# Performance work log

Measured on AMD Instinct MI355X. Metric: run time of the kernel, lower is better.

Reference implementation:

```python
import jax, jax.numpy as jnp
import numpy as np

M, N = 32, 32          # grid size (input_size)
D = 8                  # input_dim
H = 64                 # hidden_dim
O = 1                  # output_dim
B = 8                  # batch
AVG_DEG = 32           # average in-degree of the grid graph


def _build_graph_edges():
    """Host-side (numpy) construction of the sparse grid graph and edge lists,
    mirroring GraphLSTM.__construct_net: self-edge first for every node, then
    every j with graph[i, j] != 0 (after |g| < 0.5 thresholding)."""
    rng = np.random.RandomState(0)
    MN = M * N
    keep = rng.rand(MN, MN) < (AVG_DEG / MN)
    sign = rng.choice([-1.0, 1.0], size=(MN, MN))
    mag = rng.uniform(0.5, 1.0, size=(MN, MN))  # magnitudes survive threshold
    graph = np.where(keep, sign * mag, 0.0).astype(np.float32)
    graph[(-0.5 < graph) & (graph < 0.5)] = 0.0  # faithful thresholding
    dst_nz, src_nz = np.nonzero(graph)
    # self edges are always present (weight = graph[i, i], possibly 0)
    self_idx = np.arange(MN)
    dst = np.concatenate([self_idx, dst_nz]).astype(np.int32)
    src = np.concatenate([self_idx, src_nz]).astype(np.int32)
    w = np.concatenate([np.diagonal(graph), graph[dst_nz, src_nz]]).astype(np.float32)
    return dst, src, w


def setup_inputs() -> dict:
    key = jax.random.key(0)
    k_x, k_wih, k_bih, k_bhh, k_cw, k_cb = jax.random.split(key, 6)
    dst_np, src_np, w_np = _build_graph_edges()
    E = dst_np.shape[0]
    scale = 0.05
    return {
        "x": jax.random.normal(k_x, (B, D, M, N), dtype=jnp.float32),
        "edge_w": jnp.asarray(w_np),                     # (E,)
        "W_ih": jax.random.normal(k_wih, (E, 4 * H, D), dtype=jnp.float32) * scale,
        "b_ih": jax.random.normal(k_bih, (E, 4 * H), dtype=jnp.float32) * scale,
        "b_hh": jax.random.normal(k_bhh, (E, 4 * H), dtype=jnp.float32) * scale,
        "conv_w": jax.random.normal(k_cw, (O, H), dtype=jnp.float32) * scale,
        "conv_b": jax.random.normal(k_cb, (O,), dtype=jnp.float32) * scale,
        "src_idx": jnp.asarray(src_np),                  # (E,) int32
        "dst_idx": jnp.asarray(dst_np),                  # (E,) int32
    }


def reference(x, edge_w, W_ih, b_ih, b_hh, conv_w, conv_b, src_idx, dst_idx):
    Bb, Dd, Mm, Nn = x.shape
    MN = Mm * Nn
    xf = x.reshape(Bb, Dd, MN)
    # gather per-edge source features: (B, D, E)
    x_src = xf[:, :, src_idx]
    # per-edge distinct LSTM cell, single step from zero state:
    # gates = x @ W_ih^T + b_ih + (W_hh @ h0 == 0) + b_hh
    gates = jnp.einsum('bde,egd->beg', x_src, W_ih) + b_ih + b_hh  # (B, E, 4H)
    i_g, f_g, g_g, o_g = jnp.split(gates, 4, axis=-1)  # torch LSTM gate order i,f,g,o
    c_new = jax.nn.sigmoid(i_g) * jnp.tanh(g_g)        # c0 = 0 => forget path drops
    h_new = jax.nn.sigmoid(o_g) * jnp.tanh(c_new)      # (B, E, H)
    # weighted scatter-sum over destination nodes
    wh = edge_w[None, :, None] * h_new                  # (B, E, H)
    node = jax.ops.segment_sum(jnp.swapaxes(wh, 0, 1), dst_idx, num_segments=MN)  # (MN, B, H)
    frame = jnp.transpose(node, (1, 2, 0)).reshape(Bb, H, Mm, Nn)  # (B, H, M, N)
    # 1x1 conv: hidden -> output channels
    out = jnp.einsum('bhmn,oh->bomn', frame, conv_w) + conv_b[None, :, None, None]
    return out
```

## Files before the change

### kernel.cpp

```cpp
#include <hip/hip_runtime.h>
#include <hip/hip_bf16.h>


#define MN 1024
#define BB 8
#define NCOPY 32

__device__ __forceinline__ float fsig(float x) {
    return __builtin_amdgcn_rcpf(1.0f + __expf(-x));
}
__device__ __forceinline__ float ftanh(float x) {
    float t = fminf(fmaxf(2.0f * x, -30.0f), 30.0f);
    float e = __expf(t);
    return (e - 1.0f) * __builtin_amdgcn_rcpf(e + 1.0f);
}
__device__ __forceinline__ float rl(float v, int idx) {
    return __int_as_float(__builtin_amdgcn_readlane(__float_as_int(v), idx));
}

__global__ void prep_kernel(const float* __restrict__ x,
                            float* __restrict__ xt,
                            float* __restrict__ partial) {
    int tid = blockIdx.x * 256 + threadIdx.x;
    if (tid < MN * BB * 8) {
        int mn = tid >> 6;
        int b  = (tid >> 3) & 7;
        int d  = tid & 7;
        xt[tid] = x[b * (8 * MN) + d * MN + mn];
    }
    float4* p4 = (float4*)partial;
    p4[tid] = make_float4(0.f, 0.f, 0.f, 0.f);
}

__global__ void reduce_kernel(const float* __restrict__ partial,
                              const float* __restrict__ conv_b,
                              float* __restrict__ out) {
    int tid = blockIdx.x * 256 + threadIdx.x;
    float s = conv_b[0];
#pragma unroll
    for (int k = 0; k < NCOPY; ++k) s += partial[k * (BB * MN) + tid];
    out[tid] = s;
}

struct WRegs {
    float4 wi0, wi1, wg0, wg1, wo0, wo1;
    float  bIi, bIh, bGi, bGh, bOi, bOh;
};

__device__ __forceinline__ void loadW(WRegs& r, int e, int lane,
        const float* __restrict__ W, const float* __restrict__ b_ih,
        const float* __restrict__ b_hh) {
    const float* We = W + (size_t)e * 2048 + lane * 8;
    r.wi0 = *(const float4*)(We);
    r.wi1 = *(const float4*)(We + 4);
    r.wg0 = *(const float4*)(We + 1024);
    r.wg1 = *(const float4*)(We + 1028);
    r.wo0 = *(const float4*)(We + 1536);
    r.wo1 = *(const float4*)(We + 1540);
    const float* bi = b_ih + (size_t)e * 256 + lane;
    const float* bh = b_hh + (size_t)e * 256 + lane;
    r.bIi = bi[0];   r.bIh = bh[0];
    r.bGi = bi[128]; r.bGh = bh[128];
    r.bOi = bi[192]; r.bOh = bh[192];
}

__device__ __forceinline__ void computeEdge(const WRegs& r, float xreg,
        int dst, float ew, float cw, float* __restrict__ pout, int lane) {
    float bI = r.bIi + r.bIh;
    float bG = r.bGi + r.bGh;
    float bO = r.bOi + r.bOh;
    float s[BB];
#pragma unroll
    for (int b = 0; b < BB; ++b) {
        float x0 = rl(xreg, b * 8 + 0), x1 = rl(xreg, b * 8 + 1);
        float x2 = rl(xreg, b * 8 + 2), x3 = rl(xreg, b * 8 + 3);
        float x4 = rl(xreg, b * 8 + 4), x5 = rl(xreg, b * 8 + 5);
        float x6 = rl(xreg, b * 8 + 6), x7 = rl(xreg, b * 8 + 7);
        float pi = bI, pg = bG, po = bO;
        pi = fmaf(r.wi0.x, x0, pi); pg = fmaf(r.wg0.x, x0, pg); po = fmaf(r.wo0.x, x0, po);
        pi = fmaf(r.wi0.y, x1, pi); pg = fmaf(r.wg0.y, x1, pg); po = fmaf(r.wo0.y, x1, po);
        pi = fmaf(r.wi0.z, x2, pi); pg = fmaf(r.wg0.z, x2, pg); po = fmaf(r.wo0.z, x2, po);
        pi = fmaf(r.wi0.w, x3, pi); pg = fmaf(r.wg0.w, x3, pg); po = fmaf(r.wo0.w, x3, po);
        pi = fmaf(r.wi1.x, x4, pi); pg = fmaf(r.wg1.x, x4, pg); po = fmaf(r.wo1.x, x4, po);
        pi = fmaf(r.wi1.y, x5, pi); pg = fmaf(r.wg1.y, x5, pg); po = fmaf(r.wo1.y, x5, po);
        pi = fmaf(r.wi1.z, x6, pi); pg = fmaf(r.wg1.z, x6, pg); po = fmaf(r.wo1.z, x6, po);
        pi = fmaf(r.wi1.w, x7, pi); pg = fmaf(r.wg1.w, x7, pg); po = fmaf(r.wo1.w, x7, po);
        float c = fsig(pi) * ftanh(pg);
        float h = fsig(po) * ftanh(c);
        s[b] = cw * h;
    }
    float u[4];
#pragma unroll
    for (int k = 0; k < 4; ++k) {
        float keep = (lane & 32) ? s[k + 4] : s[k];
        float send = (lane & 32) ? s[k]     : s[k + 4];
        u[k] = keep + __shfl_xor(send, 32, 64);
    }
    float v[2];
#pragma unroll
    for (int k = 0; k < 2; ++k) {
        float keep = (lane & 16) ? u[k + 2] : u[k];
        float send = (lane & 16) ? u[k]     : u[k + 2];
        v[k] = keep + __shfl_xor(send, 16, 64);
    }
    float keep = (lane & 8) ? v[1] : v[0];
    float send = (lane & 8) ? v[0] : v[1];
    float t = keep + __shfl_xor(send, 8, 64);
    t += __shfl_xor(t, 4, 64);
    t += __shfl_xor(t, 2, 64);
    t += __shfl_xor(t, 1, 64);
    if ((lane & 7) == 0) {
        int b = lane >> 3;
        atomicAdd(pout + b * MN + dst, ew * t);
    }
}

__global__ __launch_bounds__(256, 4) void edge_kernel(
        const float* __restrict__ xt,
        const float* __restrict__ edge_w,
        const float* __restrict__ W,
        const float* __restrict__ b_ih,
        const float* __restrict__ b_hh,
        const float* __restrict__ conv_w,
        const int*   __restrict__ src_idx,
        const int*   __restrict__ dst_idx,
        float* __restrict__ partial,
        int E) {
    int lane = threadIdx.x & 63;
    int nw = gridDim.x * 4;
    int wid = blockIdx.x * 4 + (threadIdx.x >> 6);
    int e0 = __builtin_amdgcn_readfirstlane(wid);
    if (e0 >= E) return;
    float cw = conv_w[lane];
    float* pout = partial + (size_t)(wid & (NCOPY - 1)) * (BB * MN);

    int eC = e0, eN = e0 + nw, eN2 = eN + nw;

    int   srcC = src_idx[eC], dstC = dst_idx[eC];
    float ewC  = edge_w[eC];
    int srcN = 0, dstN = 0; float ewN = 0.0f;
    if (eN < E) { srcN = src_idx[eN]; dstN = dst_idx[eN]; ewN = edge_w[eN]; }

    WRegs A, B;
    loadW(A, eC, lane, W, b_ih, b_hh);
    float xA = xt[(size_t)srcC * 64 + lane];
    float xB = 0.0f;
    bool useA = true;

    while (true) {
        bool hasN  = (eN  < E);
        bool hasN2 = (eN2 < E);
        int srcN2 = 0, dstN2 = 0; float ewN2 = 0.0f;
        if (hasN2) { srcN2 = src_idx[eN2]; dstN2 = dst_idx[eN2]; ewN2 = edge_w[eN2]; }

        if (hasN) {
            if (useA) { loadW(B, eN, lane, W, b_ih, b_hh);
                        xB = xt[(size_t)srcN * 64 + lane]; }
            else      { loadW(A, eN, lane, W, b_ih, b_hh);
                        xA = xt[(size_t)srcN * 64 + lane]; }
        }
        __builtin_amdgcn_sched_barrier(0);

        if (useA) computeEdge(A, xA, dstC, ewC, cw, pout, lane);
        else      computeEdge(B, xB, dstC, ewC, cw, pout, lane);

        if (!hasN) break;
        srcC = srcN; dstC = dstN; ewC = ewN;
        srcN = srcN2; dstN = dstN2; ewN = ewN2;
        eC = eN; eN = eN2; eN2 += nw;
        useA = !useA;
    }
}

extern "C" void kernel_launch(void* const* d_in, const int* in_sizes, int n_in,
                              void* d_out, int out_size, void* d_ws, size_t ws_size,
                              hipStream_t stream) {
    const float* x      = (const float*)d_in[0];
    const float* edge_w = (const float*)d_in[1];
    const float* W_ih   = (const float*)d_in[2];
    const float* b_ih   = (const float*)d_in[3];
    const float* b_hh   = (const float*)d_in[4];
    const float* conv_w = (const float*)d_in[5];
    const float* conv_b = (const float*)d_in[6];
    const int* src_idx  = (const int*)d_in[7];
    const int* dst_idx  = (const int*)d_in[8];
    int E = in_sizes[1];

    float* xt      = (float*)d_ws;
    float* partial = (float*)d_ws + 65536;
    float* out     = (float*)d_out;

    prep_kernel<<<256, 256, 0, stream>>>(x, xt, partial);

    edge_kernel<<<1024, 256, 0, stream>>>(xt, edge_w, W_ih, b_ih, b_hh,
                                          conv_w, src_idx, dst_idx, partial, E);

    reduce_kernel<<<32, 256, 0, stream>>>(partial, conv_b, out);
}
```

Baseline: 63.65 us.

## Replace register double-buffering with higher occupancy and larger grid

Removes the software double-buffered weight prefetch (two WRegs sets, sched_barrier) in the edge kernel and loads each edge's weights just before computing it. The register budget drops, so launch bounds go from 4 to 6 blocks per CU and the grid grows from 1024 to 1536 blocks. Latency hiding now comes from more resident waves instead of explicit prefetch. The risk is that the exposed per-edge load latency outweighs the extra occupancy.

```diff
diff --git a/kernel.cpp b/kernel.cpp
--- a/kernel.cpp
+++ b/kernel.cpp
@@ -115,7 +115,7 @@
     }
 }
 
-__global__ __launch_bounds__(256, 4) void edge_kernel(
+__global__ __launch_bounds__(256, 6) void edge_kernel(
         const float* __restrict__ xt,
         const float* __restrict__ edge_w,
         const float* __restrict__ W,
@@ -129,46 +129,27 @@
     int lane = threadIdx.x & 63;
     int nw = gridDim.x * 4;
     int wid = blockIdx.x * 4 + (threadIdx.x >> 6);
-    int e0 = __builtin_amdgcn_readfirstlane(wid);
-    if (e0 >= E) return;
+    int e = __builtin_amdgcn_readfirstlane(wid);
+    if (e >= E) return;
     float cw = conv_w[lane];
     float* pout = partial + (size_t)(wid & (NCOPY - 1)) * (BB * MN);
 
-    int eC = e0, eN = e0 + nw, eN2 = eN + nw;
-
-    int   srcC = src_idx[eC], dstC = dst_idx[eC];
-    float ewC  = edge_w[eC];
-    int srcN = 0, dstN = 0; float ewN = 0.0f;
-    if (eN < E) { srcN = src_idx[eN]; dstN = dst_idx[eN]; ewN = edge_w[eN]; }
-
-    WRegs A, B;
-    loadW(A, eC, lane, W, b_ih, b_hh);
-    float xA = xt[(size_t)srcC * 64 + lane];
-    float xB = 0.0f;
-    bool useA = true;
+    int   srcC = src_idx[e], dstC = dst_idx[e];
+    float ewC  = edge_w[e];
 
     while (true) {
-        bool hasN  = (eN  < E);
-        bool hasN2 = (eN2 < E);
-        int srcN2 = 0, dstN2 = 0; float ewN2 = 0.0f;
-        if (hasN2) { srcN2 = src_idx[eN2]; dstN2 = dst_idx[eN2]; ewN2 = edge_w[eN2]; }
+        int eN = e + nw;
+        bool hasN = (eN < E);
+        int srcN = 0, dstN = 0; float ewN = 0.0f;
+        if (hasN) { srcN = src_idx[eN]; dstN = dst_idx[eN]; ewN = edge_w[eN]; }
 
-        if (hasN) {
-            if (useA) { loadW(B, eN, lane, W, b_ih, b_hh);
-                        xB = xt[(size_t)srcN * 64 + lane]; }
-            else      { loadW(A, eN, lane, W, b_ih, b_hh);
-                        xA = xt[(size_t)srcN * 64 + lane]; }
-        }
-        __builtin_amdgcn_sched_barrier(0);
-
-        if (useA) computeEdge(A, xA, dstC, ewC, cw, pout, lane);
-        else      computeEdge(B, xB, dstC, ewC, cw, pout, lane);
+        WRegs A;
+        loadW(A, e, lane, W, b_ih, b_hh);
+        float xA = xt[(size_t)srcC * 64 + lane];
+        computeEdge(A, xA, dstC, ewC, cw, pout, lane);
 
         if (!hasN) break;
-        srcC = srcN; dstC = dstN; ewC = ewN;
-        srcN = srcN2; dstN = dstN2; ewN = ewN2;
-        eC = eN; eN = eN2; eN2 += nw;
-        useA = !useA;
+        e = eN; srcC = srcN; dstC = dstN; ewC = ewN;
     }
 }
 
@@ -192,7 +173,7 @@
 
     prep_kernel<<<256, 256, 0, stream>>>(x, xt, partial);
 
-    edge_kernel<<<1024, 256, 0, stream>>>(xt, edge_w, W_ih, b_ih, b_hh,
+    edge_kernel<<<1536, 256, 0, stream>>>(xt, edge_w, W_ih, b_ih, b_hh,
                                           conv_w, src_idx, dst_idx, partial, E);
 
     reduce_kernel<<<32, 256, 0, stream>>>(partial, conv_b, out);
```

Result: faster. 57.65 us (-9.4%).
